# Performance work log

Hardware: AMD Instinct MI355X
Metric: run time of the kernel (lower is better)

Reference implementation:

```python
import jax, jax.numpy as jnp
import numpy as np

D_MODEL = 1024
N_HEADS = 16
D_K = D_MODEL // N_HEADS


def setup_inputs() -> dict:
    key = jax.random.key(0)
    ks = jax.random.split(key, 9)
    s = 1.0 / np.sqrt(D_MODEL)
    x = jax.random.normal(ks[0], (4, 2048, D_MODEL), dtype=jnp.float32)
    def lin(kw, kb):
        W = jax.random.uniform(kw, (D_MODEL, D_MODEL), jnp.float32, -s, s)
        b = jax.random.uniform(kb, (D_MODEL,), jnp.float32, -s, s)
        return W, b
    W_q, b_q = lin(ks[1], ks[2])
    W_k, b_k = lin(ks[3], ks[4])
    W_v, b_v = lin(ks[5], ks[6])
    W_o, b_o = lin(ks[7], ks[8])
    return {"x": x, "W_q": W_q, "b_q": b_q, "W_k": W_k, "b_k": b_k,
            "W_v": W_v, "b_v": b_v, "W_o": W_o, "b_o": b_o}


def reference(x, W_q, b_q, W_k, b_k, W_v, b_v, W_o, b_o):
    B, S, D = x.shape
    # projections: torch Linear computes x @ W.T + b
    Q = x @ W_q.T + b_q
    K = x @ W_k.T + b_k
    V = x @ W_v.T + b_v
    # split heads -> [B, H, S, d_k]
    Q = Q.reshape(B, S, N_HEADS, D_K).transpose(0, 2, 1, 3)
    K = K.reshape(B, S, N_HEADS, D_K).transpose(0, 2, 1, 3)
    V = V.reshape(B, S, N_HEADS, D_K).transpose(0, 2, 1, 3)
    scale = float(np.sqrt(D_K))
    scores = jnp.einsum('bhqd,bhkd->bhqk', Q, K) / scale
    # max-subtract + softmax == stable softmax (no mask, dropout is eval no-op)
    attn = jax.nn.softmax(scores, axis=-1)
    context = jnp.einsum('bhqk,bhkd->bhqd', attn, V)
    context = context.transpose(0, 2, 1, 3).reshape(B, S, D)
    return context @ W_o.T + b_o
```

## Files before the change

kernel.cpp:

```cpp
#include <hip/hip_runtime.h>
#include <hip/hip_bf16.h>
#include <cstdint>

#define D_MODEL 1024
#define N_HEADS 16
#define SEQ     2048
#define BATCH   4
#define M_TOT   (BATCH*SEQ)

typedef short bf16x8 __attribute__((ext_vector_type(8)));
typedef short bf16x4 __attribute__((ext_vector_type(4)));
typedef float f32x4  __attribute__((ext_vector_type(4)));
typedef __hip_bfloat16 bf16;

__device__ __forceinline__ void gld_lds16(const void* g, void* l) {
    __builtin_amdgcn_global_load_lds(
        (const __attribute__((address_space(1))) void*)(uintptr_t)g,
        (__attribute__((address_space(3))) void*)(uint32_t)(uintptr_t)l,
        16, 0, 0);
}

__global__ __launch_bounds__(256)
void cvt_all(const float* __restrict__ x,  const float* __restrict__ Wq,
             const float* __restrict__ Wk, const float* __restrict__ Wv,
             const float* __restrict__ Wo,
             bf16* __restrict__ xb, bf16* __restrict__ Wqb,
             bf16* __restrict__ Wkb, bf16* __restrict__ Wvb,
             bf16* __restrict__ Wob)
{
    const size_t CH = (size_t)1024*1024;
    int c = blockIdx.y;
    const float* src; bf16* dst;
    if (c < 8)       { src = x  + (size_t)c*CH; dst = xb  + (size_t)c*CH; }
    else if (c == 8) { src = Wq; dst = Wqb; }
    else if (c == 9) { src = Wk; dst = Wkb; }
    else if (c ==10) { src = Wv; dst = Wvb; }
    else             { src = Wo; dst = Wob; }
    int i = (blockIdx.x * 256 + threadIdx.x) * 8;
    float4 a = *(const float4*)(src + i);
    float4 b = *(const float4*)(src + i + 4);
    union { bf16 h[8]; uint4 v; } pk;
    pk.h[0] = __float2bfloat16(a.x); pk.h[1] = __float2bfloat16(a.y);
    pk.h[2] = __float2bfloat16(a.z); pk.h[3] = __float2bfloat16(a.w);
    pk.h[4] = __float2bfloat16(b.x); pk.h[5] = __float2bfloat16(b.y);
    pk.h[6] = __float2bfloat16(b.z); pk.h[7] = __float2bfloat16(b.w);
    *(uint4*)(dst + i) = pk.v;
}

template<int MODE>
__device__ __forceinline__
void gemm128_body(const bf16* __restrict__ A, const bf16* __restrict__ W,
                  const float* __restrict__ bias, void* __restrict__ Cout,
                  float scale, int m0, int n0w, int n0c, bf16* As, bf16* Bs)
{
    constexpr int K = D_MODEL, N = D_MODEL;
    const int tid  = threadIdx.x;
    const int wv   = tid >> 6;
    const int lane = tid & 63;
    const int quad = lane >> 4;
    const int l16  = lane & 15;
    const int l8   = l16 & 7;
    const int wr   = wv >> 1, wc = wv & 1;

    const int srow_off = lane >> 3;
    const int sgc      = (lane & 7) ^ srow_off;

    f32x4 acc[4][4];
    #pragma unroll
    for (int i = 0; i < 4; ++i)
        #pragma unroll
        for (int j = 0; j < 4; ++j) acc[i][j] = (f32x4){0.f,0.f,0.f,0.f};

    for (int k0 = 0; k0 < K; k0 += 64) {
        __syncthreads();
        #pragma unroll
        for (int r = 0; r < 4; ++r) {
            int row0 = wv*32 + r*8;
            gld_lds16(A + (size_t)(m0  + row0 + srow_off)*K + k0 + sgc*8,
                      As + row0*64);
            gld_lds16(W + (size_t)(n0w + row0 + srow_off)*K + k0 + sgc*8,
                      Bs + row0*64);
        }
        __syncthreads();
        #pragma unroll
        for (int ks = 0; ks < 2; ++ks) {
            bf16x8 af[4], bfb[4];
            #pragma unroll
            for (int i = 0; i < 4; ++i)
                af[i] = *(const bf16x8*)(As + (wr*64 + i*16 + l16)*64
                                         + (((ks*4 + quad) ^ l8))*8);
            #pragma unroll
            for (int j = 0; j < 4; ++j)
                bfb[j] = *(const bf16x8*)(Bs + (wc*64 + j*16 + l16)*64
                                          + (((ks*4 + quad) ^ l8))*8);
            #pragma unroll
            for (int i = 0; i < 4; ++i)
                #pragma unroll
                for (int j = 0; j < 4; ++j)
                    acc[i][j] = __builtin_amdgcn_mfma_f32_16x16x32_bf16(af[i], bfb[j], acc[i][j], 0,0,0);
        }
    }

    #pragma unroll
    for (int j = 0; j < 4; ++j) {
        int n = n0c + wc*64 + j*16 + l16;
        float bv = bias[n];
        #pragma unroll
        for (int i = 0; i < 4; ++i) {
            if constexpr (MODE == 2) {
                union { bf16 hh[4]; uint2 u; } pk;
                #pragma unroll
                for (int r = 0; r < 4; ++r)
                    pk.hh[r] = __float2bfloat16((acc[i][j][r] + bv) * scale);
                int mb = m0 + wr*64 + i*16 + quad*4;
                *(uint2*)((bf16*)Cout + (size_t)n*M_TOT + mb) = pk.u;
            } else {
                #pragma unroll
                for (int r = 0; r < 4; ++r) {
                    int m = m0 + wr*64 + i*16 + quad*4 + r;
                    float v = (acc[i][j][r] + bv) * scale;
                    if constexpr (MODE == 0)
                        ((bf16*)Cout)[(size_t)m*N + n] = __float2bfloat16(v);
                    else
                        ((float*)Cout)[(size_t)m*N + n] = v;
                }
            }
        }
    }
}

#define QSCALE (0.125f * 1.44269504089f)

__global__ __launch_bounds__(256)
void gemm_qkv(const bf16* __restrict__ xb, const bf16* __restrict__ Wcat,
              const float* __restrict__ bq, const float* __restrict__ bk,
              const float* __restrict__ bv,
              bf16* __restrict__ Qp, bf16* __restrict__ Kp, bf16* __restrict__ VT)
{
    __shared__ __attribute__((aligned(16))) bf16 As[128*64];
    __shared__ __attribute__((aligned(16))) bf16 Bs[128*64];
    const int m0 = blockIdx.x * 128, n0w = blockIdx.y * 128;
    const int sel = n0w >> 10, n0c = n0w & 1023;
    if (sel == 0)
        gemm128_body<0>(xb, Wcat, bq, Qp, QSCALE, m0, n0w, n0c, As, Bs);
    else if (sel == 1)
        gemm128_body<0>(xb, Wcat, bk, Kp, 1.0f, m0, n0w, n0c, As, Bs);
    else
        gemm128_body<2>(xb, Wcat, bv, VT, 1.0f, m0, n0w, n0c, As, Bs);
}

__global__ __launch_bounds__(256)
void gemm_out(const bf16* __restrict__ Cp, const bf16* __restrict__ Wo,
              const float* __restrict__ bo, float* __restrict__ out)
{
    __shared__ __attribute__((aligned(16))) bf16 As[128*64];
    __shared__ __attribute__((aligned(16))) bf16 Bs[128*64];
    const int n0 = blockIdx.y * 128;
    gemm128_body<1>(Cp, Wo, bo, out, 1.0f, blockIdx.x*128, n0, n0, As, Bs);
}

__global__ __launch_bounds__(256)
void flash_attn11(const bf16* __restrict__ Q, const bf16* __restrict__ Kp,
                  const bf16* __restrict__ VT, bf16* __restrict__ ctx)
{
    __shared__ __attribute__((aligned(16))) bf16 Ks[2][64*64];
    __shared__ __attribute__((aligned(16))) bf16 Vs[2][64*64];

    const int tid  = threadIdx.x;
    const int wv   = tid >> 6;
    const int lane = tid & 63;
    const int quad = lane >> 4;
    const int l16  = lane & 15;
    const int l8   = l16 & 7;

    const int b  = blockIdx.z;
    const int h  = blockIdx.y;
    const int q0 = blockIdx.x * 128;

    const bf16* kbase = Kp + (size_t)(b*SEQ)*D_MODEL + h*64;
    const bf16* vbase = VT + (size_t)(h*64)*M_TOT + (size_t)b*SEQ;

    const int srow_off = lane >> 3;
    const int sgc      = (lane & 7) ^ srow_off;

    bf16x8 aq[2][2];
    #pragma unroll
    for (int g = 0; g < 2; ++g) {
        const bf16* qp = Q + (size_t)(b*SEQ + q0 + wv*32 + g*16 + l16)*D_MODEL + h*64;
        aq[g][0] = *(const bf16x8*)(qp + quad*8);
        aq[g][1] = *(const bf16x8*)(qp + 32 + quad*8);
    }

    float l_lane[2] = {0.f, 0.f};
    f32x4 o[2][4];
    #pragma unroll
    for (int g = 0; g < 2; ++g)
        #pragma unroll
        for (int j = 0; j < 4; ++j) o[g][j] = (f32x4){0.f,0.f,0.f,0.f};

    #pragma unroll
    for (int t = 0; t < 2; ++t) {
        int row0 = wv*16 + t*8;
        gld_lds16(kbase + (size_t)(row0 + srow_off)*D_MODEL + sgc*8,
                  &Ks[0][row0*64]);
        gld_lds16(vbase + (size_t)(row0 + srow_off)*M_TOT + sgc*8,
                  &Vs[0][row0*64]);
    }

    for (int kt = 0; kt < SEQ/64; ++kt) {
        const int cur = kt & 1;
        __syncthreads();
        if (kt + 1 < SEQ/64) {
            #pragma unroll
            for (int t = 0; t < 2; ++t) {
                int row0 = wv*16 + t*8;
                gld_lds16(kbase + (size_t)((kt+1)*64 + row0 + srow_off)*D_MODEL + sgc*8,
                          &Ks[cur^1][row0*64]);
                gld_lds16(vbase + (size_t)(row0 + srow_off)*M_TOT + (kt+1)*64 + sgc*8,
                          &Vs[cur^1][row0*64]);
            }
        }

        bf16x4 paf[2][4];
        #pragma unroll
        for (int ktile = 0; ktile < 4; ++ktile) {
            bf16x8 ak[2];
            #pragma unroll
            for (int ks = 0; ks < 2; ++ks)
                ak[ks] = *(const bf16x8*)(&Ks[cur][(ktile*16 + l16)*64
                                          + ((ks*4 + quad) ^ l8)*8]);
            #pragma unroll
            for (int g = 0; g < 2; ++g) {
                f32x4 st = (f32x4){0.f,0.f,0.f,0.f};
                st = __builtin_amdgcn_mfma_f32_16x16x32_bf16(ak[0], aq[g][0], st, 0,0,0);
                st = __builtin_amdgcn_mfma_f32_16x16x32_bf16(ak[1], aq[g][1], st, 0,0,0);
                union { bf16 hh[4]; bf16x4 v; } pk;
                #pragma unroll
                for (int r = 0; r < 4; ++r) {
                    float p = __builtin_amdgcn_exp2f(st[r]);
                    l_lane[g] += p;
                    pk.hh[r] = __float2bfloat16(p);
                }
                paf[g][ktile] = pk.v;
            }
        }

        #pragma unroll
        for (int ktile = 0; ktile < 4; ++ktile)
            #pragma unroll
            for (int jt = 0; jt < 4; ++jt) {
                bf16x4 bv = *(const bf16x4*)(&Vs[cur][(jt*16 + l16)*64
                              + ((ktile*2 + (quad>>1)) ^ l8)*8 + (quad&1)*4]);
                #pragma unroll
                for (int g = 0; g < 2; ++g)
                    o[g][jt] = __builtin_amdgcn_mfma_f32_16x16x16bf16_1k(
                                   paf[g][ktile], bv, o[g][jt], 0, 0, 0);
            }
    }

    #pragma unroll
    for (int g = 0; g < 2; ++g) {
        float l = l_lane[g];
        l += __shfl_xor(l, 16);
        l += __shfl_xor(l, 32);
        #pragma unroll
        for (int r = 0; r < 4; ++r) {
            float inv = 1.f / __shfl(l, quad*4 + r, 16);
            int q = q0 + wv*32 + g*16 + quad*4 + r;
            #pragma unroll
            for (int j = 0; j < 4; ++j)
                ctx[(size_t)(b*SEQ + q)*D_MODEL + h*64 + j*16 + l16] =
                    __float2bfloat16(o[g][j][r] * inv);
        }
    }
}

extern "C" void kernel_launch(void* const* d_in, const int* in_sizes, int n_in,
                              void* d_out, int out_size, void* d_ws, size_t ws_size,
                              hipStream_t stream)
{
    const float* x  = (const float*)d_in[0];
    const float* Wq = (const float*)d_in[1];
    const float* bq = (const float*)d_in[2];
    const float* Wk = (const float*)d_in[3];
    const float* bk = (const float*)d_in[4];
    const float* Wv = (const float*)d_in[5];
    const float* bv = (const float*)d_in[6];
    const float* Wo = (const float*)d_in[7];
    const float* bo = (const float*)d_in[8];

    const size_t NEL = (size_t)M_TOT * D_MODEL;
    const size_t WEL = (size_t)D_MODEL * D_MODEL;

    bf16* ws  = (bf16*)d_ws;
    bf16* xb  = ws;
    bf16* Wqb = ws + NEL;
    bf16* Wkb = Wqb + WEL;
    bf16* Wvb = Wkb + WEL;
    bf16* Wob = Wvb + WEL;
    bf16* Qp  = Wob + WEL;
    bf16* Kp  = Qp + NEL;
    bf16* VT  = Kp + NEL;
    bf16* Cp  = VT + NEL;
    float* out = (float*)d_out;

    dim3 blk(256);
    hipLaunchKernelGGL(cvt_all, dim3(512, 12), blk, 0, stream,
                       x, Wq, Wk, Wv, Wo, xb, Wqb, Wkb, Wvb, Wob);
    hipLaunchKernelGGL(gemm_qkv, dim3(M_TOT/128, 3*D_MODEL/128), blk, 0, stream,
                       xb, Wqb, bq, bk, bv, Qp, Kp, VT);
    hipLaunchKernelGGL(flash_attn11, dim3(SEQ/128, N_HEADS, BATCH), blk, 0, stream,
                       Qp, Kp, VT, Cp);
    hipLaunchKernelGGL(gemm_out, dim3(M_TOT/128, D_MODEL/128), blk, 0, stream,
                       Cp, Wob, bo, out);
}
```

Before: 287.3 us.

## Double-buffer GEMM K-tiles and compute softmax row sums with MFMA

The projection GEMMs switch from a single 64-wide K tile with two barriers per step to double-buffered 32-wide K tiles. The next tile's global-to-LDS load is issued before computing on the current one, so one barrier per step suffices and load latency can overlap the MFMAs. In the attention kernel, the per-lane exp accumulation and end-of-kernel shuffle reduction are replaced by an extra MFMA against a vector of ones, which yields the row sums directly in the output layout. This adds MFMA work but removes the VALU adds, and it sums the bf16-rounded probabilities rather than the fp32 values.

```diff
diff --git a/kernel.cpp b/kernel.cpp
--- a/kernel.cpp
+++ b/kernel.cpp
@@ -51,7 +51,8 @@
 __device__ __forceinline__
 void gemm128_body(const bf16* __restrict__ A, const bf16* __restrict__ W,
                   const float* __restrict__ bias, void* __restrict__ Cout,
-                  float scale, int m0, int n0w, int n0c, bf16* As, bf16* Bs)
+                  float scale, int m0, int n0w, int n0c,
+                  bf16 (*As)[128*32], bf16 (*Bs)[128*32])
 {
     constexpr int K = D_MODEL, N = D_MODEL;
     const int tid  = threadIdx.x;
@@ -59,11 +60,12 @@
     const int lane = tid & 63;
     const int quad = lane >> 4;
     const int l16  = lane & 15;
-    const int l8   = l16 & 7;
     const int wr   = wv >> 1, wc = wv & 1;
 
-    const int srow_off = lane >> 3;
-    const int sgc      = (lane & 7) ^ srow_off;
+    const int srow4 = lane >> 2;
+    const int sg4   = (lane & 3) ^ (srow4 & 3);
+    const bf16* Ag = A + (size_t)(m0  + srow4)*K + sg4*8;
+    const bf16* Wg = W + (size_t)(n0w + srow4)*K + sg4*8;
 
     f32x4 acc[4][4];
     #pragma unroll
@@ -71,34 +73,38 @@
         #pragma unroll
         for (int j = 0; j < 4; ++j) acc[i][j] = (f32x4){0.f,0.f,0.f,0.f};
 
-    for (int k0 = 0; k0 < K; k0 += 64) {
+    #pragma unroll
+    for (int t = 0; t < 2; ++t) {
+        int row0 = wv*32 + t*16;
+        gld_lds16(Ag + (size_t)row0*K, As[0] + row0*32);
+        gld_lds16(Wg + (size_t)row0*K, Bs[0] + row0*32);
+    }
+
+    const int fgo = (quad ^ (l16 & 3)) * 8;
+
+    for (int k0 = 0; k0 < K; k0 += 32) {
+        const int cur = (k0 >> 5) & 1;
         __syncthreads();
-        #pragma unroll
-        for (int r = 0; r < 4; ++r) {
-            int row0 = wv*32 + r*8;
-            gld_lds16(A + (size_t)(m0  + row0 + srow_off)*K + k0 + sgc*8,
-                      As + row0*64);
-            gld_lds16(W + (size_t)(n0w + row0 + srow_off)*K + k0 + sgc*8,
-                      Bs + row0*64);
-        }
-        __syncthreads();
-        #pragma unroll
-        for (int ks = 0; ks < 2; ++ks) {
-            bf16x8 af[4], bfb[4];
-            #pragma unroll
-            for (int i = 0; i < 4; ++i)
-                af[i] = *(const bf16x8*)(As + (wr*64 + i*16 + l16)*64
-                                         + (((ks*4 + quad) ^ l8))*8);
+        if (k0 + 32 < K) {
+            #pragma unroll
+            for (int t = 0; t < 2; ++t) {
+                int row0 = wv*32 + t*16;
+                gld_lds16(Ag + (size_t)row0*K + (k0+32), As[cur^1] + row0*32);
+                gld_lds16(Wg + (size_t)row0*K + (k0+32), Bs[cur^1] + row0*32);
+            }
+        }
+        bf16x8 af[4], bfb[4];
+        #pragma unroll
+        for (int i = 0; i < 4; ++i)
+            af[i] = *(const bf16x8*)(As[cur] + (wr*64 + i*16 + l16)*32 + fgo);
+        #pragma unroll
+        for (int j = 0; j < 4; ++j)
+            bfb[j] = *(const bf16x8*)(Bs[cur] + (wc*64 + j*16 + l16)*32 + fgo);
+        #pragma unroll
+        for (int i = 0; i < 4; ++i)
             #pragma unroll
             for (int j = 0; j < 4; ++j)
-                bfb[j] = *(const bf16x8*)(Bs + (wc*64 + j*16 + l16)*64
-                                          + (((ks*4 + quad) ^ l8))*8);
-            #pragma unroll
-            for (int i = 0; i < 4; ++i)
-                #pragma unroll
-                for (int j = 0; j < 4; ++j)
-                    acc[i][j] = __builtin_amdgcn_mfma_f32_16x16x32_bf16(af[i], bfb[j], acc[i][j], 0,0,0);
-        }
+                acc[i][j] = __builtin_amdgcn_mfma_f32_16x16x32_bf16(af[i], bfb[j], acc[i][j], 0,0,0);
     }
 
     #pragma unroll
@@ -137,8 +143,8 @@
               const float* __restrict__ bv,
               bf16* __restrict__ Qp, bf16* __restrict__ Kp, bf16* __restrict__ VT)
 {
-    __shared__ __attribute__((aligned(16))) bf16 As[128*64];
-    __shared__ __attribute__((aligned(16))) bf16 Bs[128*64];
+    __shared__ __attribute__((aligned(16))) bf16 As[2][128*32];
+    __shared__ __attribute__((aligned(16))) bf16 Bs[2][128*32];
     const int m0 = blockIdx.x * 128, n0w = blockIdx.y * 128;
     const int sel = n0w >> 10, n0c = n0w & 1023;
     if (sel == 0)
@@ -153,14 +159,14 @@
 void gemm_out(const bf16* __restrict__ Cp, const bf16* __restrict__ Wo,
               const float* __restrict__ bo, float* __restrict__ out)
 {
-    __shared__ __attribute__((aligned(16))) bf16 As[128*64];
-    __shared__ __attribute__((aligned(16))) bf16 Bs[128*64];
+    __shared__ __attribute__((aligned(16))) bf16 As[2][128*32];
+    __shared__ __attribute__((aligned(16))) bf16 Bs[2][128*32];
     const int n0 = blockIdx.y * 128;
     gemm128_body<1>(Cp, Wo, bo, out, 1.0f, blockIdx.x*128, n0, n0, As, Bs);
 }
 
 __global__ __launch_bounds__(256)
-void flash_attn11(const bf16* __restrict__ Q, const bf16* __restrict__ Kp,
+void flash_attn12(const bf16* __restrict__ Q, const bf16* __restrict__ Kp,
                   const bf16* __restrict__ VT, bf16* __restrict__ ctx)
 {
     __shared__ __attribute__((aligned(16))) bf16 Ks[2][64*64];
@@ -191,12 +197,16 @@
         aq[g][1] = *(const bf16x8*)(qp + 32 + quad*8);
     }
 
-    float l_lane[2] = {0.f, 0.f};
+    const bf16x4 vones = {(short)0x3F80, (short)0x3F80, (short)0x3F80, (short)0x3F80};
+
+    f32x4 l_acc[2];
     f32x4 o[2][4];
     #pragma unroll
-    for (int g = 0; g < 2; ++g)
+    for (int g = 0; g < 2; ++g) {
+        l_acc[g] = (f32x4){0.f,0.f,0.f,0.f};
         #pragma unroll
         for (int j = 0; j < 4; ++j) o[g][j] = (f32x4){0.f,0.f,0.f,0.f};
+    }
 
     #pragma unroll
     for (int t = 0; t < 2; ++t) {
@@ -236,12 +246,11 @@
                 st = __builtin_amdgcn_mfma_f32_16x16x32_bf16(ak[1], aq[g][1], st, 0,0,0);
                 union { bf16 hh[4]; bf16x4 v; } pk;
                 #pragma unroll
-                for (int r = 0; r < 4; ++r) {
-                    float p = __builtin_amdgcn_exp2f(st[r]);
-                    l_lane[g] += p;
-                    pk.hh[r] = __float2bfloat16(p);
-                }
+                for (int r = 0; r < 4; ++r)
+                    pk.hh[r] = __float2bfloat16(__builtin_amdgcn_exp2f(st[r]));
                 paf[g][ktile] = pk.v;
+                l_acc[g] = __builtin_amdgcn_mfma_f32_16x16x16bf16_1k(
+                               paf[g][ktile], vones, l_acc[g], 0, 0, 0);
             }
         }
 
@@ -259,20 +268,16 @@
     }
 
     #pragma unroll
-    for (int g = 0; g < 2; ++g) {
-        float l = l_lane[g];
-        l += __shfl_xor(l, 16);
-        l += __shfl_xor(l, 32);
+    for (int g = 0; g < 2; ++g)
         #pragma unroll
         for (int r = 0; r < 4; ++r) {
-            float inv = 1.f / __shfl(l, quad*4 + r, 16);
+            float inv = 1.f / l_acc[g][r];
             int q = q0 + wv*32 + g*16 + quad*4 + r;
             #pragma unroll
             for (int j = 0; j < 4; ++j)
                 ctx[(size_t)(b*SEQ + q)*D_MODEL + h*64 + j*16 + l16] =
                     __float2bfloat16(o[g][j][r] * inv);
         }
-    }
 }
 
 extern "C" void kernel_launch(void* const* d_in, const int* in_sizes, int n_in,
@@ -309,7 +314,7 @@
                        x, Wq, Wk, Wv, Wo, xb, Wqb, Wkb, Wvb, Wob);
     hipLaunchKernelGGL(gemm_qkv, dim3(M_TOT/128, 3*D_MODEL/128), blk, 0, stream,
                        xb, Wqb, bq, bk, bv, Qp, Kp, VT);
-    hipLaunchKernelGGL(flash_attn11, dim3(SEQ/128, N_HEADS, BATCH), blk, 0, stream,
+    hipLaunchKernelGGL(flash_attn12, dim3(SEQ/128, N_HEADS, BATCH), blk, 0, stream,
                        Qp, Kp, VT, Cp);
     hipLaunchKernelGGL(gemm_out, dim3(M_TOT/128, D_MODEL/128), blk, 0, stream,
                        Cp, Wob, bo, out);
```

Measured after the change: 287.5 us. No clear change (+0.1%).
